# Kernel optimization log

Hardware: AMD Instinct MI355X
Metric: run time of the kernel (lower is better)

Reference implementation:

```python
import jax, jax.numpy as jnp
import numpy as np

M, N, D, H, R = 16384, 32, 128, 8, 237
Dh = D // H
SCALE = Dh ** -0.5
LN_EPS = 1e-5


def setup_inputs() -> dict:
    key = jax.random.key(0)
    ks = jax.random.split(key, 12)
    entity_repr = jax.random.normal(ks[0], (M, D), dtype=jnp.float32)
    neighbor_index = jax.random.randint(ks[1], (M, N), 0, M, dtype=jnp.int64)
    rel_ids = jax.random.randint(ks[2], (M, N), 0, R, dtype=jnp.int64)
    neighbor_mask = jax.random.randint(ks[3], (M, N), 0, 2, dtype=jnp.int32).astype(bool)
    neighbor_mask = neighbor_mask.at[:, 0].set(True)  # ensure >=1 valid neighbor per node
    s = 1.0 / np.sqrt(D)
    # weights stored in right-multiply form: y = x @ W + b
    Wq = jax.random.normal(ks[4], (D, D), dtype=jnp.float32) * s
    Wk = jax.random.normal(ks[5], (D, D), dtype=jnp.float32) * s
    Wv = jax.random.normal(ks[6], (D, D), dtype=jnp.float32) * s
    Wo = jax.random.normal(ks[7], (D, D), dtype=jnp.float32) * s
    bq = jnp.zeros((D,), jnp.float32)
    bk = jnp.zeros((D,), jnp.float32)
    bv = jnp.zeros((D,), jnp.float32)
    bo = jnp.zeros((D,), jnp.float32)
    rel_table = jax.random.normal(ks[8], (R, D), dtype=jnp.float32)
    ln_gamma = jnp.ones((D,), jnp.float32)
    ln_beta = jnp.zeros((D,), jnp.float32)
    return {
        "entity_repr": entity_repr, "neighbor_index": neighbor_index,
        "rel_ids": rel_ids, "neighbor_mask": neighbor_mask,
        "Wq": Wq, "bq": bq, "Wk": Wk, "bk": bk, "Wv": Wv, "bv": bv,
        "Wo": Wo, "bo": bo, "rel_table": rel_table,
        "ln_gamma": ln_gamma, "ln_beta": ln_beta,
    }


def _layernorm(x, gamma, beta):
    mu = jnp.mean(x, axis=-1, keepdims=True)
    var = jnp.var(x, axis=-1, keepdims=True)
    return (x - mu) * jax.lax.rsqrt(var + LN_EPS) * gamma + beta


def reference(entity_repr, neighbor_index, rel_ids, neighbor_mask,
              Wq, bq, Wk, bk, Wv, bv, Wo, bo, rel_table, ln_gamma, ln_beta):
    valid = neighbor_mask
    safe_index = jnp.where(valid, neighbor_index, 0)
    safe_rel = jnp.where(valid, rel_ids, 0)
    neighbor_repr = entity_repr[safe_index]          # [M, N, D] irregular gather
    rel_emb = rel_table[safe_rel]                     # [M, N, D]
    q = (entity_repr @ Wq + bq).reshape(M, H, Dh)     # [M, H, Dh] (query len 1)
    k = ((neighbor_repr + rel_emb) @ Wk + bk).reshape(M, N, H, Dh)
    v = (neighbor_repr @ Wv + bv).reshape(M, N, H, Dh)
    attn = jnp.einsum("mhd,mnhd->mhn", q, k) * SCALE  # [M, H, N]
    attn = jnp.where(valid[:, None, :], attn, -jnp.inf)
    attn = jax.nn.softmax(attn, axis=-1)
    attn = jnp.nan_to_num(attn, nan=0.0)
    out = jnp.einsum("mhn,mnhd->mhd", attn, v).reshape(M, D)
    out = out @ Wo + bo
    return _layernorm(entity_repr + out, ln_gamma, ln_beta)
```

## Files before the change

### kernel.cpp

```cpp
#include <hip/hip_runtime.h>

#define M_NODES 16384
#define NNBR 32
#define RREL 237
#define ATTN_SCALE 0.25f
#define LN_EPS 1e-5f

typedef float float4v __attribute__((ext_vector_type(4)));
typedef unsigned int uint4v __attribute__((ext_vector_type(4)));
typedef short short8 __attribute__((ext_vector_type(8)));
typedef float floatx4 __attribute__((ext_vector_type(4)));

__device__ __forceinline__ float bfu2f(unsigned short u) {
    return __builtin_bit_cast(float, ((unsigned int)u) << 16);
}
__device__ __forceinline__ unsigned short f2bfu(float f) {
    unsigned int x = __builtin_bit_cast(unsigned int, f);
    unsigned int lsb = (x >> 16) & 1u;
    x += 0x7fffu + lsb;
    return (unsigned short)(x >> 16);
}
__device__ __forceinline__ unsigned int pack2(float a, float b) {
    return (unsigned int)f2bfu(a) | ((unsigned int)f2bfu(b) << 16);
}
__device__ __forceinline__ float unpk_lo(unsigned int u) {
    return __builtin_bit_cast(float, u << 16);
}
__device__ __forceinline__ float unpk_hi(unsigned int u) {
    return __builtin_bit_cast(float, u & 0xffff0000u);
}


__global__ __launch_bounds__(256) void prep_w(
    const float* __restrict__ Wq, const float* __restrict__ Wk,
    const float* __restrict__ Wv, const float* __restrict__ Wo,
    const float* __restrict__ entity,
    const int* __restrict__ nidx, const int* __restrict__ nrel,
    const int* __restrict__ nmask,
    unsigned short* __restrict__ WqT, unsigned short* __restrict__ WkT,
    unsigned short* __restrict__ WvT, unsigned short* __restrict__ WoT,
    unsigned short* __restrict__ Eb, unsigned int* __restrict__ PIX) {
    int t = threadIdx.x;
    if (blockIdx.x < 32) {
        int mat  = blockIdx.x >> 3;
        int slab = blockIdx.x & 7;
        const float* W = (mat == 0) ? Wq : (mat == 1) ? Wk : (mat == 2) ? Wv : Wo;
        unsigned short* WT = (mat == 0) ? WqT : (mat == 1) ? WkT : (mat == 2) ? WvT : WoT;
        #pragma unroll
        for (int i = 0; i < 8; ++i) {
            int idx = t + 256 * i;
            int r = slab * 16 + (idx >> 7);
            int c = idx & 127;
            WT[c * 128 + r] = f2bfu(W[r * 128 + c]);
        }
    } else if (blockIdx.x < 160) {
        int b = blockIdx.x - 32;
        const float* src = entity + (size_t)b * 16384;
        unsigned short* dst = Eb + (size_t)b * 16384;
        #pragma unroll
        for (int i = 0; i < 8; ++i) {
            int o = (i * 256 + t) * 8;
            float4v f0 = *(const float4v*)&src[o];
            float4v f1 = *(const float4v*)&src[o + 4];
            short8 s;
            #pragma unroll
            for (int j = 0; j < 4; ++j) {
                s[j]     = (short)f2bfu(f0[j]);
                s[4 + j] = (short)f2bfu(f1[j]);
            }
            *(short8*)&dst[o] = s;
        }
    } else {
        int base = (blockIdx.x - 160) * 8192;
        #pragma unroll 8
        for (int i = 0; i < 32; ++i) {
            int e = base + i * 256 + t;
            int mk = nmask[e];
            int ix = nidx[e];
            int ir = nrel[e];
            if (!mk) { ix = 0; ir = 0; }
            ix = ix < 0 ? 0 : (ix > M_NODES - 1 ? M_NODES - 1 : ix);
            ir = ir < 0 ? 0 : (ir > RREL - 1 ? RREL - 1 : ir);
            PIX[e] = (unsigned)ix | ((unsigned)ir << 14) | (mk ? 0x80000000u : 0u);
        }
    }
}

__global__ __launch_bounds__(256) void gemm4_mfma(
    const float* __restrict__ rel_table, const unsigned short* __restrict__ Eb,
    const unsigned short* __restrict__ WqT, const unsigned short* __restrict__ WkT,
    const unsigned short* __restrict__ WvT,
    const float* __restrict__ bq, const float* __restrict__ bk,
    const float* __restrict__ bv,
    unsigned short* __restrict__ EQb, unsigned short* __restrict__ EKV,
    unsigned short* __restrict__ RKb) {
    __shared__ __align__(16) unsigned short lw[128 * 136];

    int y = blockIdx.y;
    const unsigned short* WT; const float* bias; int arows;
    unsigned short* outb; int ostride, ooff;
    if (y == 0)      { WT = WqT; bias = bq;      arows = M_NODES; outb = EQb; ostride = 128; ooff = 0;   }
    else if (y == 1) { WT = WkT; bias = nullptr; arows = M_NODES; outb = EKV; ostride = 256; ooff = 0;   }
    else if (y == 2) { WT = WvT; bias = bv;      arows = M_NODES; outb = EKV; ostride = 256; ooff = 128; }
    else             { WT = WkT; bias = bk;      arows = RREL;    outb = RKb; ostride = 128; ooff = 0;   }

    int rbase = blockIdx.x * 64;
    if (rbase >= arows) return;
    int t = threadIdx.x;
    int wave = t >> 6, lane = t & 63;
    int lm = lane & 15, quad = lane >> 4;
    int m0 = rbase + wave * 16;
    int r0 = m0 + lm; if (r0 >= arows) r0 = arows - 1;

    short8 af[4];
    if (y == 3) {
        #pragma unroll
        for (int ks = 0; ks < 4; ++ks) {
            int koff = ks * 32 + quad * 8;
            float4v f0 = *(const float4v*)&rel_table[r0 * 128 + koff];
            float4v f1 = *(const float4v*)&rel_table[r0 * 128 + koff + 4];
            #pragma unroll
            for (int j = 0; j < 4; ++j) {
                af[ks][j]     = (short)f2bfu(f0[j]);
                af[ks][4 + j] = (short)f2bfu(f1[j]);
            }
        }
    } else {
        #pragma unroll
        for (int ks = 0; ks < 4; ++ks)
            af[ks] = *(const short8*)&Eb[r0 * 128 + ks * 32 + quad * 8];
    }

    #pragma unroll
    for (int i = 0; i < 8; ++i) {
        int ci = t + 256 * i;
        int r  = ci >> 4;
        int c8 = ci & 15;
        *(short8*)&lw[r * 136 + c8 * 8] = *(const short8*)&WT[r * 128 + c8 * 8];
    }
    __syncthreads();

    floatx4 acc[8];
    #pragma unroll
    for (int c = 0; c < 8; ++c) acc[c] = (floatx4){0.f, 0.f, 0.f, 0.f};

    #pragma unroll
    for (int ks = 0; ks < 4; ++ks) {
        int koff = ks * 32 + quad * 8;
        #pragma unroll
        for (int c = 0; c < 8; ++c) {
            short8 b = *(const short8*)&lw[(c * 16 + lm) * 136 + koff];
            acc[c] = __builtin_amdgcn_mfma_f32_16x16x32_bf16(af[ks], b, acc[c], 0, 0, 0);
        }
    }

    #pragma unroll
    for (int c = 0; c < 8; ++c) {
        int col = c * 16 + lm;
        float bb = bias ? bias[col] : 0.0f;
        int rb = m0 + quad * 4;
        #pragma unroll
        for (int j = 0; j < 4; ++j) {
            int r = rb + j;
            if (r < arows) outb[r * ostride + ooff + col] = f2bfu(acc[c][j] + bb);
        }
    }
}

__global__ __launch_bounds__(256, 7) void attn_gather(
    const unsigned int* __restrict__ PIX,
    const unsigned short* __restrict__ EQb, const unsigned short* __restrict__ EKV,
    const unsigned short* __restrict__ RKb,
    unsigned short* __restrict__ OATb) {
    __shared__ float Pl[4][8][33];

    int w = threadIdx.x >> 6, l = threadIdx.x & 63;
    int m = blockIdx.x * 4 + w;
    int lm = l & 15, quad = l >> 4;
    int n0 = l & 31;

    unsigned pix = PIX[m * NNBR + n0];

    short8 q8v[4];
    #pragma unroll
    for (int ks = 0; ks < 4; ++ks)
        q8v[ks] = *(const short8*)&EQb[m * 128 + ks * 32 + quad * 8];

    int ix = (int)(pix & 0x3FFFu);
    int ir = (int)((pix >> 14) & 0xFFu);
    unsigned long long bal = __ballot((pix >> 31) != 0);
    unsigned maskbits = (unsigned)(bal & 0xffffffffu);

    int rowK0 = __shfl(ix, lm, 64),      rowK1 = __shfl(ix, 16 + lm, 64);
    int rowR0 = __shfl(ir, lm, 64),      rowR1 = __shfl(ir, 16 + lm, 64);

    floatx4 acc0 = (floatx4){0.f, 0.f, 0.f, 0.f};
    floatx4 acc1 = (floatx4){0.f, 0.f, 0.f, 0.f};
    const short8 zero8 = (short8){0, 0, 0, 0, 0, 0, 0, 0};
    #pragma unroll
    for (int ks = 0; ks < 4; ++ks) {
        int koff = ks * 32 + quad * 8;
        int h = ks * 2 + (quad >> 1);
        short8 bq = (lm == h) ? q8v[ks] : zero8;
        short8 k0 = *(const short8*)&EKV[rowK0 * 256 + koff];
        short8 k1 = *(const short8*)&EKV[rowK1 * 256 + koff];
        short8 r0 = *(const short8*)&RKb[rowR0 * 128 + koff];
        short8 r1 = *(const short8*)&RKb[rowR1 * 128 + koff];
        acc0 = __builtin_amdgcn_mfma_f32_16x16x32_bf16(k0, bq, acc0, 0, 0, 0);
        acc0 = __builtin_amdgcn_mfma_f32_16x16x32_bf16(r0, bq, acc0, 0, 0, 0);
        acc1 = __builtin_amdgcn_mfma_f32_16x16x32_bf16(k1, bq, acc1, 0, 0, 0);
        acc1 = __builtin_amdgcn_mfma_f32_16x16x32_bf16(r1, bq, acc1, 0, 0, 0);
    }

    uint4v vreg[8];
    #pragma unroll
    for (int i = 0; i < 8; ++i) {
        int ixx = __shfl(ix, quad + i * 4, 64);
        vreg[i] = *(const uint4v*)&EKV[ixx * 256 + 128 + lm * 8];
    }

    float lf[2][4];
    #pragma unroll
    for (int j = 0; j < 4; ++j) {
        int na = quad * 4 + j, nb = 16 + quad * 4 + j;
        float va = acc0[j] * ATTN_SCALE;
        float vb = acc1[j] * ATTN_SCALE;
        lf[0][j] = ((maskbits >> na) & 1) ? va : -1e30f;
        lf[1][j] = ((maskbits >> nb) & 1) ? vb : -1e30f;
    }
    float mx = -1e30f;
    #pragma unroll
    for (int g = 0; g < 2; ++g)
        #pragma unroll
        for (int j = 0; j < 4; ++j) mx = fmaxf(mx, lf[g][j]);
    mx = fmaxf(mx, __shfl_xor(mx, 16, 64));
    mx = fmaxf(mx, __shfl_xor(mx, 32, 64));
    float p[2][4];
    float s = 0.f;
    #pragma unroll
    for (int g = 0; g < 2; ++g)
        #pragma unroll
        for (int j = 0; j < 4; ++j) { p[g][j] = __expf(lf[g][j] - mx); s += p[g][j]; }
    s += __shfl_xor(s, 16, 64);
    s += __shfl_xor(s, 32, 64);
    float inv = 1.0f / s;
    if (lm < 8) {
        #pragma unroll
        for (int g = 0; g < 2; ++g)
            #pragma unroll
            for (int j = 0; j < 4; ++j)
                Pl[w][lm][g * 16 + quad * 4 + j] = p[g][j] * inv;
    }

    float o[8] = {0.f, 0.f, 0.f, 0.f, 0.f, 0.f, 0.f, 0.f};
    #pragma unroll
    for (int i = 0; i < 8; ++i) {
        float pp = Pl[w][lm >> 1][quad + i * 4];
        uint4v v = vreg[i];
        #pragma unroll
        for (int k = 0; k < 4; ++k) {
            o[2 * k]     += pp * unpk_lo(v[k]);
            o[2 * k + 1] += pp * unpk_hi(v[k]);
        }
    }
    #pragma unroll
    for (int j = 0; j < 8; ++j) {
        o[j] += __shfl_xor(o[j], 16, 64);
        o[j] += __shfl_xor(o[j], 32, 64);
    }
    if (quad == 0) {
        uint4v u;
        u[0] = pack2(o[0], o[1]); u[1] = pack2(o[2], o[3]);
        u[2] = pack2(o[4], o[5]); u[3] = pack2(o[6], o[7]);
        *(uint4v*)&OATb[m * 128 + lm * 8] = u;
    }
}

__global__ __launch_bounds__(256) void gemm_wo_ln(
    const unsigned short* __restrict__ OATb, const unsigned short* __restrict__ WoT,
    const float* __restrict__ bo, const float* __restrict__ entity,
    const float* __restrict__ gamma_, const float* __restrict__ beta_,
    float* __restrict__ OUT) {
    __shared__ __align__(16) unsigned short lw[128 * 136];

    int t = threadIdx.x;
    int wave = t >> 6, lane = t & 63;
    int lm = lane & 15, quad = lane >> 4;
    int m0 = blockIdx.x * 64 + wave * 16;
    int r0 = m0 + lm;

    short8 af[4];
    #pragma unroll
    for (int ks = 0; ks < 4; ++ks)
        af[ks] = *(const short8*)&OATb[r0 * 128 + ks * 32 + quad * 8];

    #pragma unroll
    for (int i = 0; i < 8; ++i) {
        int ci = t + 256 * i;
        int r  = ci >> 4;
        int c8 = ci & 15;
        *(short8*)&lw[r * 136 + c8 * 8] = *(const short8*)&WoT[r * 128 + c8 * 8];
    }
    __syncthreads();

    floatx4 acc[8];
    #pragma unroll
    for (int c = 0; c < 8; ++c) acc[c] = (floatx4){0.f, 0.f, 0.f, 0.f};

    #pragma unroll
    for (int ks = 0; ks < 4; ++ks) {
        int koff = ks * 32 + quad * 8;
        #pragma unroll
        for (int c = 0; c < 8; ++c) {
            short8 b = *(const short8*)&lw[(c * 16 + lm) * 136 + koff];
            acc[c] = __builtin_amdgcn_mfma_f32_16x16x32_bf16(af[ks], b, acc[c], 0, 0, 0);
        }
    }

    float bb[8], gg[8], be[8];
    #pragma unroll
    for (int c = 0; c < 8; ++c) {
        int col = c * 16 + lm;
        bb[c] = bo[col]; gg[c] = gamma_[col]; be[c] = beta_[col];
    }
    #pragma unroll
    for (int j = 0; j < 4; ++j) {
        int r = m0 + quad * 4 + j;
        float y[8];
        float s1 = 0.f, s2 = 0.f;
        #pragma unroll
        for (int c = 0; c < 8; ++c) {
            float v = acc[c][j] + bb[c] + entity[r * 128 + c * 16 + lm];
            y[c] = v; s1 += v; s2 += v * v;
        }
        #pragma unroll
        for (int off = 8; off >= 1; off >>= 1) {
            s1 += __shfl_xor(s1, off, 16);
            s2 += __shfl_xor(s2, off, 16);
        }
        float mu  = s1 * (1.0f / 128.0f);
        float var = fmaxf(s2 * (1.0f / 128.0f) - mu * mu, 0.0f);
        float rs  = rsqrtf(var + LN_EPS);
        #pragma unroll
        for (int c = 0; c < 8; ++c)
            OUT[r * 128 + c * 16 + lm] = (y[c] - mu) * rs * gg[c] + be[c];
    }
}

__global__ __launch_bounds__(256, 6) void rga_fused(
    const float* __restrict__ entity,
    const int* __restrict__ nidx,
    const int* __restrict__ nrel,
    const int* __restrict__ nmask,
    const float* __restrict__ Wq, const float* __restrict__ bq,
    const float* __restrict__ Wk, const float* __restrict__ bk,
    const float* __restrict__ Wv, const float* __restrict__ bv,
    const float* __restrict__ Wo, const float* __restrict__ bo,
    const float* __restrict__ rel_table,
    const float* __restrict__ gamma_, const float* __restrict__ beta_,
    float* __restrict__ outp) {
    __shared__ __align__(16) float er[128];
    __shared__ __align__(16) float qv[128];
    __shared__ float qb[8];
    __shared__ __align__(16) float qk[8 * 132];
    __shared__ __align__(16) unsigned int nbvp[32 * 68];
    __shared__ float Lg[8][33];
    __shared__ __align__(16) float pv[8 * 132];
    __shared__ __align__(16) float oat[128];
    __shared__ float ypart[2][128];
    __shared__ float red[4];
    __shared__ int midx[32], mrel[32], mmask[32];

    int m = blockIdx.x;
    int t = threadIdx.x;

    if (t < 32) {
        int mk = nmask[m * NNBR + t];
        int ix = nidx[m * NNBR + t];
        int ir = nrel[m * NNBR + t];
        if (!mk) { ix = 0; ir = 0; }
        ix = ix < 0 ? 0 : (ix > M_NODES - 1 ? M_NODES - 1 : ix);
        ir = ir < 0 ? 0 : (ir > RREL - 1 ? RREL - 1 : ir);
        mmask[t] = mk; midx[t] = ix; mrel[t] = ir;
    }
    if (t >= 128) er[t - 128] = entity[m * 128 + (t - 128)];
    __syncthreads();

    {
        int half = t >> 7, d = t & 127, j0 = half * 64;
        const float4v* e4 = (const float4v*)&er[j0];
        float acc = 0.f;
        #pragma unroll 4
        for (int c = 0; c < 16; ++c) {
            float4v ev = e4[c];
            #pragma unroll
            for (int k = 0; k < 4; ++k)
                acc += ev[k] * Wq[(j0 + c * 4 + k) * 128 + d];
        }
        ypart[half][d] = acc;
    }
    __syncthreads();
    if (t < 128) qv[t] = ypart[0][t] + ypart[1][t] + bq[t];
    __syncthreads();

    #pragma unroll
    for (int rep = 0; rep < 4; ++rep) {
        int o = rep * 256 + t;
        int h = o >> 7, j = o & 127;
        const float4v* wr = (const float4v*)&Wk[j * 128 + h * 16];
        const float4v* q4 = (const float4v*)&qv[h * 16];
        float s = 0.f;
        #pragma unroll
        for (int c = 0; c < 4; ++c) {
            float4v ww = wr[c], q = q4[c];
            #pragma unroll
            for (int k = 0; k < 4; ++k) s += ww[k] * q[k];
        }
        qk[h * 132 + j] = s;
    }
    if (t < 8) {
        float s = 0.f;
        #pragma unroll
        for (int dh = 0; dh < 16; ++dh) s += qv[t * 16 + dh] * bk[t * 16 + dh];
        qb[t] = s;
    }
    __syncthreads();

    {
        int n = t >> 3, c16 = t & 7, j0 = c16 * 16;
        int ix = midx[n], ir = mrel[n];
        const float4v* ep = (const float4v*)&entity[ix * 128 + j0];
        const float4v* rp = (const float4v*)&rel_table[ir * 128 + j0];
        float ev[16], kv[16];
        #pragma unroll
        for (int c = 0; c < 4; ++c) {
            float4v e4 = ep[c], r4 = rp[c];
            #pragma unroll
            for (int k = 0; k < 4; ++k) {
                ev[c * 4 + k] = e4[k];
                kv[c * 4 + k] = e4[k] + r4[k];
            }
        }
        uint4v u0, u1;
        #pragma unroll
        for (int k = 0; k < 4; ++k) u0[k] = pack2(ev[2 * k], ev[2 * k + 1]);
        #pragma unroll
        for (int k = 0; k < 4; ++k) u1[k] = pack2(ev[8 + 2 * k], ev[9 + 2 * k]);
        *(uint4v*)&nbvp[n * 68 + c16 * 8]     = u0;
        *(uint4v*)&nbvp[n * 68 + c16 * 8 + 4] = u1;
        float acc[8];
        #pragma unroll
        for (int h = 0; h < 8; ++h) {
            const float4v* qrow = (const float4v*)&qk[h * 132 + j0];
            float s = 0.f;
            #pragma unroll
            for (int c = 0; c < 4; ++c) {
                float4v q = qrow[c];
                #pragma unroll
                for (int k = 0; k < 4; ++k) s += q[k] * kv[c * 4 + k];
            }
            acc[h] = s;
        }
        #pragma unroll
        for (int off = 1; off < 8; off <<= 1) {
            #pragma unroll
            for (int h = 0; h < 8; ++h) acc[h] += __shfl_xor(acc[h], off, 8);
        }
        if (c16 == 0) {
            #pragma unroll
            for (int h = 0; h < 8; ++h) {
                float lf = (acc[h] + qb[h]) * ATTN_SCALE;
                if (!mmask[n]) lf = -1e30f;
                Lg[h][n] = lf;
            }
        }
    }
    __syncthreads();

    {
        int h = t >> 5, n = t & 31;
        float lf = Lg[h][n];
        float mx = lf;
        #pragma unroll
        for (int off = 16; off >= 1; off >>= 1) mx = fmaxf(mx, __shfl_xor(mx, off, 32));
        float p = __expf(lf - mx);
        float s = p;
        #pragma unroll
        for (int off = 16; off >= 1; off >>= 1) s += __shfl_xor(s, off, 32);
        Lg[h][n] = p / s;
    }
    __syncthreads();

    {
        int h = t >> 5, c4 = t & 31;
        float4v a = (float4v){0.f, 0.f, 0.f, 0.f};
        #pragma unroll 8
        for (int n = 0; n < 32; ++n) {
            float p = Lg[h][n];
            unsigned int w0 = nbvp[n * 68 + c4 * 2];
            unsigned int w1 = nbvp[n * 68 + c4 * 2 + 1];
            a[0] += p * unpk_lo(w0);
            a[1] += p * unpk_hi(w0);
            a[2] += p * unpk_lo(w1);
            a[3] += p * unpk_hi(w1);
        }
        *(float4v*)&pv[h * 132 + c4 * 4] = a;
    }
    __syncthreads();

    {
        int half = t >> 7, d = t & 127, j0 = half * 64;
        int h = d >> 4;
        const float4v* p4 = (const float4v*)&pv[h * 132 + j0];
        float acc = 0.f;
        #pragma unroll 4
        for (int c = 0; c < 16; ++c) {
            float4v p = p4[c];
            #pragma unroll
            for (int k = 0; k < 4; ++k)
                acc += p[k] * Wv[(j0 + c * 4 + k) * 128 + d];
        }
        ypart[half][d] = acc;
    }
    __syncthreads();
    if (t < 128) oat[t] = ypart[0][t] + ypart[1][t] + bv[t];
    __syncthreads();

    {
        int half = t >> 7, d = t & 127, j0 = half * 64;
        const float4v* o4 = (const float4v*)&oat[j0];
        float acc = 0.f;
        #pragma unroll 4
        for (int c = 0; c < 16; ++c) {
            float4v o = o4[c];
            #pragma unroll
            for (int k = 0; k < 4; ++k)
                acc += o[k] * Wo[(j0 + c * 4 + k) * 128 + d];
        }
        ypart[half][d] = acc;
    }
    __syncthreads();

    float x = 0.f;
    if (t < 128) {
        x = er[t] + ypart[0][t] + ypart[1][t] + bo[t];
        float s1 = x, s2 = x * x;
        #pragma unroll
        for (int off = 32; off >= 1; off >>= 1) {
            s1 += __shfl_xor(s1, off, 64);
            s2 += __shfl_xor(s2, off, 64);
        }
        if ((t & 63) == 0) { red[(t >> 6) * 2] = s1; red[(t >> 6) * 2 + 1] = s2; }
    }
    __syncthreads();
    if (t < 128) {
        float mu  = (red[0] + red[2]) * (1.0f / 128.0f);
        float ms  = (red[1] + red[3]) * (1.0f / 128.0f);
        float var = fmaxf(ms - mu * mu, 0.0f);
        float rs  = rsqrtf(var + LN_EPS);
        outp[m * 128 + t] = (x - mu) * rs * gamma_[t] + beta_[t];
    }
}

extern "C" void kernel_launch(void* const* d_in, const int* in_sizes, int n_in,
                              void* d_out, int out_size, void* d_ws, size_t ws_size,
                              hipStream_t stream) {
    const float* entity    = (const float*)d_in[0];
    const int*   nidx      = (const int*)d_in[1];
    const int*   nrel      = (const int*)d_in[2];
    const int*   nmask     = (const int*)d_in[3];
    const float* Wq        = (const float*)d_in[4];
    const float* bq        = (const float*)d_in[5];
    const float* Wk        = (const float*)d_in[6];
    const float* bk        = (const float*)d_in[7];
    const float* Wv        = (const float*)d_in[8];
    const float* bv        = (const float*)d_in[9];
    const float* Wo        = (const float*)d_in[10];
    const float* bo        = (const float*)d_in[11];
    const float* rel_table = (const float*)d_in[12];
    const float* gamma_    = (const float*)d_in[13];
    const float* beta_     = (const float*)d_in[14];

    char* ws = (char*)d_ws;
    unsigned short* EKV  = (unsigned short*)(ws + 0);
    unsigned short* EQb  = (unsigned short*)(ws + 8388608);
    unsigned short* OATb = (unsigned short*)(ws + 12582912);
    unsigned short* RKb  = (unsigned short*)(ws + 16777216);
    unsigned short* WqT  = (unsigned short*)(ws + 16837888);
    unsigned short* WkT  = (unsigned short*)(ws + 16870656);
    unsigned short* WvT  = (unsigned short*)(ws + 16903424);
    unsigned short* WoT  = (unsigned short*)(ws + 16936192);
    unsigned short* Eb   = (unsigned short*)(ws + 16968960);
    unsigned int*   PIX  = (unsigned int*)(ws + 21163264);
    const size_t NEED = 21163264 + 2097152;

    if (ws_size >= NEED) {
        prep_w<<<dim3(224), 256, 0, stream>>>(Wq, Wk, Wv, Wo, entity,
                                              nidx, nrel, nmask,
                                              WqT, WkT, WvT, WoT, Eb, PIX);
        gemm4_mfma<<<dim3(256, 4), 256, 0, stream>>>(
            rel_table, Eb, WqT, WkT, WvT, bq, bk, bv, EQb, EKV, RKb);
        attn_gather<<<dim3(M_NODES / 4), 256, 0, stream>>>(
            PIX, EQb, EKV, RKb, OATb);
        gemm_wo_ln<<<dim3(256), 256, 0, stream>>>(
            OATb, WoT, bo, entity, gamma_, beta_, (float*)d_out);
    } else {
        rga_fused<<<dim3(M_NODES), 256, 0, stream>>>(
            entity, nidx, nrel, nmask, Wq, bq, Wk, bk, Wv, bv, Wo, bo,
            rel_table, gamma_, beta_, (float*)d_out);
    }
}
```

Measured before the change: 136.8 us.

## Split each node's 32 neighbors across two waves in attention gather

Each node in the attention-gather kernel is now handled by two waves, each covering 16 neighbors, instead of one wave covering all 32. The waves exchange the softmax max, the softmax sum and the partial outputs through shared memory with block-wide barriers, and the grid doubles in size. The goal is more waves in flight and fewer outstanding gathers per wave, which should hide gather latency better. The cost is three __syncthreads per block plus extra shared-memory traffic, and each MFMA now does less work per wave.

```diff
diff --git a/kernel.cpp b/kernel.cpp
--- a/kernel.cpp
+++ b/kernel.cpp
@@ -172,14 +172,18 @@
     const unsigned short* __restrict__ EQb, const unsigned short* __restrict__ EKV,
     const unsigned short* __restrict__ RKb,
     unsigned short* __restrict__ OATb) {
-    __shared__ float Pl[4][8][33];
+    __shared__ float Pl[2][8][34];
+    __shared__ float Mx[2][2][16];
+    __shared__ float Sx[2][2][16];
+    __shared__ float Ox[2][16][8];
 
     int w = threadIdx.x >> 6, l = threadIdx.x & 63;
-    int m = blockIdx.x * 4 + w;
+    int nib = w >> 1;
+    int g = w & 1;
+    int m = blockIdx.x * 2 + nib;
     int lm = l & 15, quad = l >> 4;
-    int n0 = l & 31;
-
-    unsigned pix = PIX[m * NNBR + n0];
+
+    unsigned pix = PIX[m * NNBR + g * 16 + lm];
 
     short8 q8v[4];
     #pragma unroll
@@ -189,73 +193,62 @@
     int ix = (int)(pix & 0x3FFFu);
     int ir = (int)((pix >> 14) & 0xFFu);
     unsigned long long bal = __ballot((pix >> 31) != 0);
-    unsigned maskbits = (unsigned)(bal & 0xffffffffu);
-
-    int rowK0 = __shfl(ix, lm, 64),      rowK1 = __shfl(ix, 16 + lm, 64);
-    int rowR0 = __shfl(ir, lm, 64),      rowR1 = __shfl(ir, 16 + lm, 64);
-
-    floatx4 acc0 = (floatx4){0.f, 0.f, 0.f, 0.f};
-    floatx4 acc1 = (floatx4){0.f, 0.f, 0.f, 0.f};
+    unsigned maskbits = (unsigned)(bal & 0xFFFFu);
+
+    floatx4 acc = (floatx4){0.f, 0.f, 0.f, 0.f};
     const short8 zero8 = (short8){0, 0, 0, 0, 0, 0, 0, 0};
     #pragma unroll
     for (int ks = 0; ks < 4; ++ks) {
         int koff = ks * 32 + quad * 8;
         int h = ks * 2 + (quad >> 1);
         short8 bq = (lm == h) ? q8v[ks] : zero8;
-        short8 k0 = *(const short8*)&EKV[rowK0 * 256 + koff];
-        short8 k1 = *(const short8*)&EKV[rowK1 * 256 + koff];
-        short8 r0 = *(const short8*)&RKb[rowR0 * 128 + koff];
-        short8 r1 = *(const short8*)&RKb[rowR1 * 128 + koff];
-        acc0 = __builtin_amdgcn_mfma_f32_16x16x32_bf16(k0, bq, acc0, 0, 0, 0);
-        acc0 = __builtin_amdgcn_mfma_f32_16x16x32_bf16(r0, bq, acc0, 0, 0, 0);
-        acc1 = __builtin_amdgcn_mfma_f32_16x16x32_bf16(k1, bq, acc1, 0, 0, 0);
-        acc1 = __builtin_amdgcn_mfma_f32_16x16x32_bf16(r1, bq, acc1, 0, 0, 0);
-    }
-
-    uint4v vreg[8];
-    #pragma unroll
-    for (int i = 0; i < 8; ++i) {
+        short8 k0 = *(const short8*)&EKV[ix * 256 + koff];
+        short8 r0 = *(const short8*)&RKb[ir * 128 + koff];
+        acc = __builtin_amdgcn_mfma_f32_16x16x32_bf16(k0, bq, acc, 0, 0, 0);
+        acc = __builtin_amdgcn_mfma_f32_16x16x32_bf16(r0, bq, acc, 0, 0, 0);
+    }
+
+    uint4v vreg[4];
+    #pragma unroll
+    for (int i = 0; i < 4; ++i) {
         int ixx = __shfl(ix, quad + i * 4, 64);
         vreg[i] = *(const uint4v*)&EKV[ixx * 256 + 128 + lm * 8];
     }
 
-    float lf[2][4];
+    float lf[4];
     #pragma unroll
     for (int j = 0; j < 4; ++j) {
-        int na = quad * 4 + j, nb = 16 + quad * 4 + j;
-        float va = acc0[j] * ATTN_SCALE;
-        float vb = acc1[j] * ATTN_SCALE;
-        lf[0][j] = ((maskbits >> na) & 1) ? va : -1e30f;
-        lf[1][j] = ((maskbits >> nb) & 1) ? vb : -1e30f;
-    }
-    float mx = -1e30f;
-    #pragma unroll
-    for (int g = 0; g < 2; ++g)
-        #pragma unroll
-        for (int j = 0; j < 4; ++j) mx = fmaxf(mx, lf[g][j]);
+        int n = quad * 4 + j;
+        float v = acc[j] * ATTN_SCALE;
+        lf[j] = ((maskbits >> n) & 1) ? v : -1e30f;
+    }
+    float mx = fmaxf(fmaxf(lf[0], lf[1]), fmaxf(lf[2], lf[3]));
     mx = fmaxf(mx, __shfl_xor(mx, 16, 64));
     mx = fmaxf(mx, __shfl_xor(mx, 32, 64));
-    float p[2][4];
+    if (quad == 0) Mx[nib][g][lm] = mx;
+    __syncthreads();
+    float gmx = fmaxf(mx, Mx[nib][g ^ 1][lm]);
+
+    float p[4];
     float s = 0.f;
     #pragma unroll
-    for (int g = 0; g < 2; ++g)
-        #pragma unroll
-        for (int j = 0; j < 4; ++j) { p[g][j] = __expf(lf[g][j] - mx); s += p[g][j]; }
+    for (int j = 0; j < 4; ++j) { p[j] = __expf(lf[j] - gmx); s += p[j]; }
     s += __shfl_xor(s, 16, 64);
     s += __shfl_xor(s, 32, 64);
-    float inv = 1.0f / s;
+    if (quad == 0) Sx[nib][g][lm] = s;
+    __syncthreads();
+    float inv = 1.0f / (s + Sx[nib][g ^ 1][lm]);
+
     if (lm < 8) {
         #pragma unroll
-        for (int g = 0; g < 2; ++g)
-            #pragma unroll
-            for (int j = 0; j < 4; ++j)
-                Pl[w][lm][g * 16 + quad * 4 + j] = p[g][j] * inv;
+        for (int j = 0; j < 4; ++j)
+            Pl[nib][lm][g * 16 + quad * 4 + j] = p[j] * inv;
     }
 
     float o[8] = {0.f, 0.f, 0.f, 0.f, 0.f, 0.f, 0.f, 0.f};
     #pragma unroll
-    for (int i = 0; i < 8; ++i) {
-        float pp = Pl[w][lm >> 1][quad + i * 4];
+    for (int i = 0; i < 4; ++i) {
+        float pp = Pl[nib][lm >> 1][g * 16 + quad + i * 4];
         uint4v v = vreg[i];
         #pragma unroll
         for (int k = 0; k < 4; ++k) {
@@ -268,10 +261,19 @@
         o[j] += __shfl_xor(o[j], 16, 64);
         o[j] += __shfl_xor(o[j], 32, 64);
     }
-    if (quad == 0) {
+    if (g == 1 && quad == 0) {
+        #pragma unroll
+        for (int j = 0; j < 8; ++j) Ox[nib][lm][j] = o[j];
+    }
+    __syncthreads();
+    if (g == 0 && quad == 0) {
         uint4v u;
-        u[0] = pack2(o[0], o[1]); u[1] = pack2(o[2], o[3]);
-        u[2] = pack2(o[4], o[5]); u[3] = pack2(o[6], o[7]);
+        float f0 = o[0] + Ox[nib][lm][0], f1 = o[1] + Ox[nib][lm][1];
+        float f2 = o[2] + Ox[nib][lm][2], f3 = o[3] + Ox[nib][lm][3];
+        float f4 = o[4] + Ox[nib][lm][4], f5 = o[5] + Ox[nib][lm][5];
+        float f6 = o[6] + Ox[nib][lm][6], f7 = o[7] + Ox[nib][lm][7];
+        u[0] = pack2(f0, f1); u[1] = pack2(f2, f3);
+        u[2] = pack2(f4, f5); u[3] = pack2(f6, f7);
         *(uint4v*)&OATb[m * 128 + lm * 8] = u;
     }
 }
@@ -600,7 +602,7 @@
                                               WqT, WkT, WvT, WoT, Eb, PIX);
         gemm4_mfma<<<dim3(256, 4), 256, 0, stream>>>(
             rel_table, Eb, WqT, WkT, WvT, bq, bk, bv, EQb, EKV, RKb);
-        attn_gather<<<dim3(M_NODES / 4), 256, 0, stream>>>(
+        attn_gather<<<dim3(M_NODES / 2), 256, 0, stream>>>(
             PIX, EQb, EKV, RKb, OATb);
         gemm_wo_ln<<<dim3(256), 256, 0, stream>>>(
             OATb, WoT, bo, entity, gamma_, beta_, (float*)d_out);
```

Measured after the change: 140.7 us. 1.03x slower.
